# Kernel optimization log

Hardware: AMD Instinct MI355X
Metric: run time of the kernel (lower is better)

## Reference

```python
import jax, jax.numpy as jnp
import numpy as np

B, C, W, H = 4, 64, 64, 64
CQK = C // 8  # query/key channels


def setup_inputs() -> dict:
    key = jax.random.key(0)
    ks = jax.random.split(key, 8)
    s = 0.05
    return {
        "x": jax.random.normal(ks[0], (B, C, W, H), jnp.float32),
        "Wq": jax.random.normal(ks[1], (CQK, C), jnp.float32) * s,
        "bq": jax.random.normal(ks[2], (CQK,), jnp.float32) * s,
        "Wk": jax.random.normal(ks[3], (CQK, C), jnp.float32) * s,
        "bk": jax.random.normal(ks[4], (CQK,), jnp.float32) * s,
        "Wv": jax.random.normal(ks[5], (C, C), jnp.float32) * s,
        "bv": jax.random.normal(ks[6], (C,), jnp.float32) * s,
        # torch init is zeros; use a nonzero value so the attention path is exercised
        "gamma": jax.random.normal(ks[7], (1,), jnp.float32) * s,
    }


def reference(x, Wq, bq, Wk, bk, Wv, bv, gamma):
    b, c, w, h = x.shape
    n = w * h
    xf = x.reshape(b, c, n)  # B, C, N
    # 1x1 convs == per-pixel linear maps
    q = jnp.einsum("oc,bcn->bno", Wq, xf) + bq           # B, N, Cqk
    k = jnp.einsum("oc,bcn->bon", Wk, xf) + bk[:, None]   # B, Cqk, N
    energy = jnp.einsum("bno,bom->bnm", q, k)             # B, N, N
    attn = jax.nn.softmax(energy, axis=-1)                # B, N, N
    v = jnp.einsum("oc,bcn->bon", Wv, xf) + bv[:, None]   # B, C, N
    # out[b,c,j] = sum_n v[b,c,n] * attn[j,n]  (bmm with attention^T)
    out = jnp.einsum("bcn,bjn->bcj", v, attn)
    out = out.reshape(b, c, w, h)
    return gamma * out + x
```

## Files before the change

kernel.cpp:

```cpp
#include <hip/hip_runtime.h>

typedef short s16x8 __attribute__((ext_vector_type(8)));
typedef float f32x4 __attribute__((ext_vector_type(4)));
typedef float f32x16 __attribute__((ext_vector_type(16)));
typedef unsigned u32x4 __attribute__((ext_vector_type(4)));

#define BB 4
#define NN 4096
#define LOG2E 1.4426950408889634f

__device__ __forceinline__ unsigned short f2bf(float f) {
    unsigned int u = __builtin_bit_cast(unsigned int, f);
    u += 0x7fff + ((u >> 16) & 1);
    return (unsigned short)(u >> 16);
}

__device__ __forceinline__ unsigned pk2(float lo, float hi) {
    return __builtin_amdgcn_perm(__builtin_bit_cast(unsigned, hi),
                                 __builtin_bit_cast(unsigned, lo), 0x07060302u);
}

__device__ __forceinline__ void pl32swap(unsigned &a, unsigned &b) {
    asm volatile("v_permlane32_swap_b32 %0, %1" : "+v"(a), "+v"(b));
}

__global__ __launch_bounds__(256) void proj_kernel(
    const float* __restrict__ x,
    const float* __restrict__ Wq, const float* __restrict__ bq,
    const float* __restrict__ Wk, const float* __restrict__ bk,
    const float* __restrict__ Wv, const float* __restrict__ bv,
    unsigned short* __restrict__ Qw, unsigned short* __restrict__ Kw,
    unsigned short* __restrict__ Vc)
{
    __shared__ __attribute__((aligned(16))) unsigned short sW[80 * 72];
    __shared__ __attribute__((aligned(16))) unsigned short xT[64 * 72];
    __shared__ float sb[80];

    int tid = threadIdx.x;
    int p   = blockIdx.x;
    int xcd = p & 7;
    int b   = xcd >> 1;
    int nb  = ((p >> 3) << 1) | (xcd & 1);
    int n0  = nb << 6;

    for (int i = tid; i < 1280; i += 256) {
        int o = i >> 4, c4 = (i & 15) << 2;
        const float* src = (o < 8) ? &Wq[o * 64 + c4]
                         : ((o < 16) ? &Wk[(o - 8) * 64 + c4]
                                     : &Wv[(o - 16) * 64 + c4]);
        float4 v = *(const float4*)src;
        float sc = (o < 8) ? LOG2E : 1.f;
        sW[o * 72 + c4 + 0] = f2bf(v.x * sc);
        sW[o * 72 + c4 + 1] = f2bf(v.y * sc);
        sW[o * 72 + c4 + 2] = f2bf(v.z * sc);
        sW[o * 72 + c4 + 3] = f2bf(v.w * sc);
    }
    if (tid < 80)
        sb[tid] = (tid < 8) ? bq[tid] * LOG2E
                            : ((tid < 16) ? bk[tid - 8] : bv[tid - 16]);
    for (int i = tid; i < 1024; i += 256) {
        int c = i >> 4, p4 = (i & 15) << 2;
        float4 v = *(const float4*)&x[(((size_t)b * 64 + c) << 12) + n0 + p4];
        xT[(p4 + 0) * 72 + c] = f2bf(v.x);
        xT[(p4 + 1) * 72 + c] = f2bf(v.y);
        xT[(p4 + 2) * 72 + c] = f2bf(v.z);
        xT[(p4 + 3) * 72 + c] = f2bf(v.w);
    }
    __syncthreads();

    int w = tid >> 6, l = tid & 63, g = l >> 4, q16 = l & 15;
    int pix = w * 16 + q16;

    s16x8 bf0 = *(const s16x8*)&xT[pix * 72 + g * 8];
    s16x8 bf1 = *(const s16x8*)&xT[pix * 72 + 32 + g * 8];

    s16x8 a0[5], a1[5];
#pragma unroll
    for (int ot = 0; ot < 5; ++ot) {
        a0[ot] = *(const s16x8*)&sW[(ot * 16 + q16) * 72 + g * 8];
        a1[ot] = *(const s16x8*)&sW[(ot * 16 + q16) * 72 + 32 + g * 8];
    }
    __syncthreads();

    unsigned short* sV = xT;
    size_t base16 = ((size_t)(b << 12) + n0 + pix) << 4;

#pragma unroll
    for (int ot = 0; ot < 5; ++ot) {
        f32x4 acc = {0.f, 0.f, 0.f, 0.f};
        acc = __builtin_amdgcn_mfma_f32_16x16x32_bf16(a0[ot], bf0, acc, 0, 0, 0);
        acc = __builtin_amdgcn_mfma_f32_16x16x32_bf16(a1[ot], bf1, acc, 0, 0, 0);
#pragma unroll
        for (int r = 0; r < 4; ++r) {
            int orow = ot * 16 + g * 4 + r;
            unsigned short hv = f2bf(acc[r] + sb[orow]);
            if (ot == 0) {
                if (orow < 8) {
                    Qw[base16 + orow] = hv;
                    Qw[base16 + orow + 8] = 0;
                } else {
                    Kw[base16 + orow - 8] = hv;
                    Kw[base16 + orow] = 0;
                }
            } else {
                sV[(orow - 16) * 72 + pix] = hv;
            }
        }
    }
    __syncthreads();

#pragma unroll
    for (int i = tid; i < 512; i += 256) {
        int jj = i >> 6, c = i & 63;
        u32x4 v = *(const u32x4*)&sV[c * 72 + jj * 8];
        int jglob = (nb << 3) + jj;
        *(u32x4*)&Vc[(((size_t)b * 512 + jglob) * 64 + c) * 8] = v;
    }
}

__global__ __launch_bounds__(512, 2) void attn_kernel(
    const unsigned short* __restrict__ Qw, const unsigned short* __restrict__ Kw,
    const unsigned short* __restrict__ Vc, const float* __restrict__ x,
    const float* __restrict__ gamma, float* __restrict__ outp)
{
    __shared__ __attribute__((aligned(16))) float sO[64 * 36];
    __shared__ float sL[8 * 32];
    __shared__ float sGL[32];

    int tid = threadIdx.x;
    int w = tid >> 6, l = tid & 63, r31 = l & 31, hi = l >> 5;
    int p = blockIdx.x;
    int xcd = p & 7, kgrp = p >> 3;
    int b = xcd >> 1;
    int n32 = (kgrp & 1) | ((xcd & 1) << 1) | ((kgrp >> 1) << 2);
    int n0 = n32 << 5;
    float gm = gamma[0];

    s16x8 qf = *(const s16x8*)((const char*)Qw + ((size_t)b << 17)
                               + ((size_t)(n0 + r31) << 5) + (hi << 4));
    const char* KbW = (const char*)Kw + ((size_t)b << 17) + (w << 14)
                    + (r31 << 5) + (hi << 4);
    const char* VcB = (const char*)Vc + ((size_t)b << 19) + (w << 16)
                    + (hi << 10) + (r31 << 4);

    f32x16 zz;
#pragma unroll
    for (int i = 0; i < 16; ++i) zz[i] = 0.f;

    f32x16 acc0, acc1;
#pragma unroll
    for (int i = 0; i < 16; ++i) { acc0[i] = 0.f; acc1[i] = 0.f; }
    float la = 0.f;

    s16x8 cK  = *(const s16x8*)(KbW);
    s16x8 cA0 = *(const s16x8*)(VcB);
    s16x8 cA1 = *(const s16x8*)(VcB + 2048);
    s16x8 cB0 = *(const s16x8*)(VcB + 512);
    s16x8 cB1 = *(const s16x8*)(VcB + 2560);

#pragma unroll
    for (int ch = 0; ch < 16; ++ch) {
        s16x8 nK = cK, nA0 = cA0, nA1 = cA1, nB0 = cB0, nB1 = cB1;
        if (ch < 15) {
            const char* pk = KbW + ((ch + 1) << 10);
            const char* pv = VcB + ((ch + 1) << 12);
            nK  = *(const s16x8*)(pk);
            nA0 = *(const s16x8*)(pv);
            nA1 = *(const s16x8*)(pv + 2048);
            nB0 = *(const s16x8*)(pv + 512);
            nB1 = *(const s16x8*)(pv + 2560);
        }

        f32x16 E = __builtin_amdgcn_mfma_f32_32x32x16_bf16(cK, qf, zz, 0, 0, 0);
#pragma unroll
        for (int i = 0; i < 16; ++i) E[i] = __builtin_amdgcn_exp2f(E[i]);
        la += (((E[0] + E[1]) + (E[2] + E[3])) + ((E[4] + E[5]) + (E[6] + E[7])))
            + (((E[8] + E[9]) + (E[10] + E[11])) + ((E[12] + E[13]) + (E[14] + E[15])));

        unsigned x0 = pk2(E[0], E[1]),   x1 = pk2(E[2], E[3]);
        unsigned x2 = pk2(E[4], E[5]),   x3 = pk2(E[6], E[7]);
        unsigned x4 = pk2(E[8], E[9]),   x5 = pk2(E[10], E[11]);
        unsigned x6 = pk2(E[12], E[13]), x7 = pk2(E[14], E[15]);
        pl32swap(x0, x2); pl32swap(x1, x3);
        pl32swap(x4, x6); pl32swap(x5, x7);
        u32x4 u0 = {x0, x1, x2, x3}, u1 = {x4, x5, x6, x7};
        s16x8 pf0 = __builtin_bit_cast(s16x8, u0);
        s16x8 pf1 = __builtin_bit_cast(s16x8, u1);

        acc0 = __builtin_amdgcn_mfma_f32_32x32x16_bf16(cA0, pf0, acc0, 0, 0, 0);
        acc0 = __builtin_amdgcn_mfma_f32_32x32x16_bf16(cA1, pf1, acc0, 0, 0, 0);
        acc1 = __builtin_amdgcn_mfma_f32_32x32x16_bf16(cB0, pf0, acc1, 0, 0, 0);
        acc1 = __builtin_amdgcn_mfma_f32_32x32x16_bf16(cB1, pf1, acc1, 0, 0, 0);

        cK = nK; cA0 = nA0; cA1 = nA1; cB0 = nB0; cB1 = nB1;
    }

    la += __shfl_xor(la, 32);
    if (l < 32) sL[w * 32 + l] = la;

#pragma unroll
    for (int s = 0; s < 8; ++s) {
        __syncthreads();
#pragma unroll
        for (int B = 0; B < 8; ++B) {
            if (((w + s) & 7) == B) {
                const int R2 = B & 3;
                float e0 = (B < 4) ? acc0[R2 * 4 + 0] : acc1[R2 * 4 + 0];
                float e1 = (B < 4) ? acc0[R2 * 4 + 1] : acc1[R2 * 4 + 1];
                float e2 = (B < 4) ? acc0[R2 * 4 + 2] : acc1[R2 * 4 + 2];
                float e3 = (B < 4) ? acc0[R2 * 4 + 3] : acc1[R2 * 4 + 3];
                float* pp = &sO[(B * 8 + hi * 4) * 36 + r31];
                if (s == 0) {
                    pp[0] = e0; pp[36] = e1; pp[72] = e2; pp[108] = e3;
                } else {
                    pp[0] += e0; pp[36] += e1; pp[72] += e2; pp[108] += e3;
                }
            }
        }
    }
    __syncthreads();

    if (tid < 32) {
        float L = 0.f;
#pragma unroll
        for (int wk2 = 0; wk2 < 8; ++wk2) L += sL[wk2 * 32 + tid];
        sGL[tid] = gm / L;
    }
    __syncthreads();

    {
        int c = tid >> 3, qc = tid & 7;
        float4 o4 = *(const float4*)&sO[c * 36 + qc * 4];
        float4 g4 = *(const float4*)&sGL[qc * 4];
        size_t idx = (((size_t)b * 64 + c) << 12) + n0 + qc * 4;
        float4 x4v = *(const float4*)&x[idx];
        o4.x = o4.x * g4.x + x4v.x;
        o4.y = o4.y * g4.y + x4v.y;
        o4.z = o4.z * g4.z + x4v.z;
        o4.w = o4.w * g4.w + x4v.w;
        *(float4*)&outp[idx] = o4;
    }
}

extern "C" void kernel_launch(void* const* d_in, const int* in_sizes, int n_in,
                              void* d_out, int out_size, void* d_ws, size_t ws_size,
                              hipStream_t stream) {
    const float* x     = (const float*)d_in[0];
    const float* Wq    = (const float*)d_in[1];
    const float* bq    = (const float*)d_in[2];
    const float* Wk    = (const float*)d_in[3];
    const float* bk    = (const float*)d_in[4];
    const float* Wv    = (const float*)d_in[5];
    const float* bv    = (const float*)d_in[6];
    const float* gamma = (const float*)d_in[7];
    float* out = (float*)d_out;

    unsigned short* Qw = (unsigned short*)d_ws;
    unsigned short* Kw = Qw + (size_t)BB * NN * 16;
    unsigned short* Vc = Kw + (size_t)BB * NN * 16;

    proj_kernel<<<256, 256, 0, stream>>>(x, Wq, bq, Wk, bk, Wv, bv, Qw, Kw, Vc);
    attn_kernel<<<512, 512, 0, stream>>>(Qw, Kw, Vc, x, gamma, out);
}
```

Before: 29.35 us.

## Switch attention to 16-query tiles with 16x16x32 MFMA and more blocks

Each attention block now handles 16 queries instead of 32, using 16x16x32 bf16 MFMAs and doubling the grid to 1024 blocks. Launch bounds move to 6 blocks per CU, and the loop is no longer unrolled or software-prefetched. The goal is more parallelism and occupancy so latency is hidden by other waves rather than explicit prefetch. The cost is that K/V are re-read twice as often per query, and QK MFMAs waste three quarters of their lanes on zero-padded Q/K fragments.

```diff
diff --git a/kernel.cpp b/kernel.cpp
--- a/kernel.cpp
+++ b/kernel.cpp
@@ -2,7 +2,6 @@
 
 typedef short s16x8 __attribute__((ext_vector_type(8)));
 typedef float f32x4 __attribute__((ext_vector_type(4)));
-typedef float f32x16 __attribute__((ext_vector_type(16)));
 typedef unsigned u32x4 __attribute__((ext_vector_type(4)));
 
 #define BB 4
@@ -18,10 +17,6 @@
 __device__ __forceinline__ unsigned pk2(float lo, float hi) {
     return __builtin_amdgcn_perm(__builtin_bit_cast(unsigned, hi),
                                  __builtin_bit_cast(unsigned, lo), 0x07060302u);
-}
-
-__device__ __forceinline__ void pl32swap(unsigned &a, unsigned &b) {
-    asm volatile("v_permlane32_swap_b32 %0, %1" : "+v"(a), "+v"(b));
 }
 
 __global__ __launch_bounds__(256) void proj_kernel(
@@ -118,127 +113,115 @@
     }
 }
 
-__global__ __launch_bounds__(512, 2) void attn_kernel(
+__global__ __launch_bounds__(512, 6) void attn_kernel(
     const unsigned short* __restrict__ Qw, const unsigned short* __restrict__ Kw,
     const unsigned short* __restrict__ Vc, const float* __restrict__ x,
     const float* __restrict__ gamma, float* __restrict__ outp)
 {
-    __shared__ __attribute__((aligned(16))) float sO[64 * 36];
-    __shared__ float sL[8 * 32];
-    __shared__ float sGL[32];
+    __shared__ __attribute__((aligned(16))) float sO[64 * 17];
+    __shared__ float sL[8 * 16];
+    __shared__ float sGL[16];
 
     int tid = threadIdx.x;
-    int w = tid >> 6, l = tid & 63, r31 = l & 31, hi = l >> 5;
+    int w = tid >> 6, l = tid & 63, g = l >> 4, q16 = l & 15;
     int p = blockIdx.x;
-    int xcd = p & 7, kgrp = p >> 3;
+    int xcd = p & 7;
     int b = xcd >> 1;
-    int n32 = (kgrp & 1) | ((xcd & 1) << 1) | ((kgrp >> 1) << 2);
-    int n0 = n32 << 5;
+    int hi5 = (p >> 3) >> 2, lo2 = (p >> 3) & 3;
+    int qg = (hi5 << 3) | ((xcd & 1) << 2) | lo2;
+    int n0 = qg << 4;
     float gm = gamma[0];
 
-    s16x8 qf = *(const s16x8*)((const char*)Qw + ((size_t)b << 17)
-                               + ((size_t)(n0 + r31) << 5) + (hi << 4));
-    const char* KbW = (const char*)Kw + ((size_t)b << 17) + (w << 14)
-                    + (r31 << 5) + (hi << 4);
-    const char* VcB = (const char*)Vc + ((size_t)b << 19) + (w << 16)
-                    + (hi << 10) + (r31 << 4);
-
-    f32x16 zz;
-#pragma unroll
-    for (int i = 0; i < 16; ++i) zz[i] = 0.f;
-
-    f32x16 acc0, acc1;
-#pragma unroll
-    for (int i = 0; i < 16; ++i) { acc0[i] = 0.f; acc1[i] = 0.f; }
+    s16x8 z8 = {0, 0, 0, 0, 0, 0, 0, 0};
+    f32x4 z4 = {0.f, 0.f, 0.f, 0.f};
+
+    s16x8 qf = z8;
+    if (g == 0)
+        qf = *(const s16x8*)((const char*)Qw + ((size_t)b << 17)
+                             + ((size_t)(n0 + q16) << 5));
+
+    const char* Kb = (const char*)Kw + ((size_t)b << 17) + (w << 14)
+                   + ((((q16 >> 2) << 3) + (q16 & 3)) << 5);
+    const char* Vb = (const char*)Vc + ((size_t)b << 19) + (w << 16)
+                   + (g << 10) + (q16 << 4);
+
+    f32x4 acc0 = z4, acc1 = z4, acc2 = z4, acc3 = z4;
     float la = 0.f;
 
-    s16x8 cK  = *(const s16x8*)(KbW);
-    s16x8 cA0 = *(const s16x8*)(VcB);
-    s16x8 cA1 = *(const s16x8*)(VcB + 2048);
-    s16x8 cB0 = *(const s16x8*)(VcB + 512);
-    s16x8 cB1 = *(const s16x8*)(VcB + 2560);
-
-#pragma unroll
+#pragma unroll 1
     for (int ch = 0; ch < 16; ++ch) {
-        s16x8 nK = cK, nA0 = cA0, nA1 = cA1, nB0 = cB0, nB1 = cB1;
-        if (ch < 15) {
-            const char* pk = KbW + ((ch + 1) << 10);
-            const char* pv = VcB + ((ch + 1) << 12);
-            nK  = *(const s16x8*)(pk);
-            nA0 = *(const s16x8*)(pv);
-            nA1 = *(const s16x8*)(pv + 2048);
-            nB0 = *(const s16x8*)(pv + 512);
-            nB1 = *(const s16x8*)(pv + 2560);
+        const char* kc = Kb + (ch << 10);
+        s16x8 kf0 = z8, kf1 = z8;
+        if (g == 0) {
+            kf0 = *(const s16x8*)(kc);
+            kf1 = *(const s16x8*)(kc + 128);
         }
-
-        f32x16 E = __builtin_amdgcn_mfma_f32_32x32x16_bf16(cK, qf, zz, 0, 0, 0);
-#pragma unroll
-        for (int i = 0; i < 16; ++i) E[i] = __builtin_amdgcn_exp2f(E[i]);
-        la += (((E[0] + E[1]) + (E[2] + E[3])) + ((E[4] + E[5]) + (E[6] + E[7])))
-            + (((E[8] + E[9]) + (E[10] + E[11])) + ((E[12] + E[13]) + (E[14] + E[15])));
-
-        unsigned x0 = pk2(E[0], E[1]),   x1 = pk2(E[2], E[3]);
-        unsigned x2 = pk2(E[4], E[5]),   x3 = pk2(E[6], E[7]);
-        unsigned x4 = pk2(E[8], E[9]),   x5 = pk2(E[10], E[11]);
-        unsigned x6 = pk2(E[12], E[13]), x7 = pk2(E[14], E[15]);
-        pl32swap(x0, x2); pl32swap(x1, x3);
-        pl32swap(x4, x6); pl32swap(x5, x7);
-        u32x4 u0 = {x0, x1, x2, x3}, u1 = {x4, x5, x6, x7};
-        s16x8 pf0 = __builtin_bit_cast(s16x8, u0);
-        s16x8 pf1 = __builtin_bit_cast(s16x8, u1);
-
-        acc0 = __builtin_amdgcn_mfma_f32_32x32x16_bf16(cA0, pf0, acc0, 0, 0, 0);
-        acc0 = __builtin_amdgcn_mfma_f32_32x32x16_bf16(cA1, pf1, acc0, 0, 0, 0);
-        acc1 = __builtin_amdgcn_mfma_f32_32x32x16_bf16(cB0, pf0, acc1, 0, 0, 0);
-        acc1 = __builtin_amdgcn_mfma_f32_32x32x16_bf16(cB1, pf1, acc1, 0, 0, 0);
-
-        cK = nK; cA0 = nA0; cA1 = nA1; cB0 = nB0; cB1 = nB1;
-    }
-
+        const char* vc = Vb + (ch << 12);
+        s16x8 vf0 = *(const s16x8*)(vc);
+        s16x8 vf1 = *(const s16x8*)(vc + 256);
+        s16x8 vf2 = *(const s16x8*)(vc + 512);
+        s16x8 vf3 = *(const s16x8*)(vc + 768);
+
+        f32x4 E0 = __builtin_amdgcn_mfma_f32_16x16x32_bf16(kf0, qf, z4, 0, 0, 0);
+        f32x4 E1 = __builtin_amdgcn_mfma_f32_16x16x32_bf16(kf1, qf, z4, 0, 0, 0);
+#pragma unroll
+        for (int i = 0; i < 4; ++i) E0[i] = __builtin_amdgcn_exp2f(E0[i]);
+#pragma unroll
+        for (int i = 0; i < 4; ++i) E1[i] = __builtin_amdgcn_exp2f(E1[i]);
+        la += ((E0[0] + E0[1]) + (E0[2] + E0[3]))
+            + ((E1[0] + E1[1]) + (E1[2] + E1[3]));
+
+        u32x4 uu = { pk2(E0[0], E0[1]), pk2(E0[2], E0[3]),
+                     pk2(E1[0], E1[1]), pk2(E1[2], E1[3]) };
+        s16x8 pf = __builtin_bit_cast(s16x8, uu);
+
+        acc0 = __builtin_amdgcn_mfma_f32_16x16x32_bf16(vf0, pf, acc0, 0, 0, 0);
+        acc1 = __builtin_amdgcn_mfma_f32_16x16x32_bf16(vf1, pf, acc1, 0, 0, 0);
+        acc2 = __builtin_amdgcn_mfma_f32_16x16x32_bf16(vf2, pf, acc2, 0, 0, 0);
+        acc3 = __builtin_amdgcn_mfma_f32_16x16x32_bf16(vf3, pf, acc3, 0, 0, 0);
+    }
+
+    la += __shfl_xor(la, 16);
     la += __shfl_xor(la, 32);
-    if (l < 32) sL[w * 32 + l] = la;
+    if (l < 16) sL[w * 16 + l] = la;
 
 #pragma unroll
     for (int s = 0; s < 8; ++s) {
         __syncthreads();
 #pragma unroll
         for (int B = 0; B < 8; ++B) {
-            if (((w + s) & 7) == B) {
-                const int R2 = B & 3;
-                float e0 = (B < 4) ? acc0[R2 * 4 + 0] : acc1[R2 * 4 + 0];
-                float e1 = (B < 4) ? acc0[R2 * 4 + 1] : acc1[R2 * 4 + 1];
-                float e2 = (B < 4) ? acc0[R2 * 4 + 2] : acc1[R2 * 4 + 2];
-                float e3 = (B < 4) ? acc0[R2 * 4 + 3] : acc1[R2 * 4 + 3];
-                float* pp = &sO[(B * 8 + hi * 4) * 36 + r31];
+            if (((w + s) & 7) == B && ((g >> 1) == (B & 1))) {
+                const int CT = B >> 1;
+                f32x4 e = (CT == 0) ? acc0 : ((CT == 1) ? acc1
+                        : ((CT == 2) ? acc2 : acc3));
+                float* pp = &sO[(CT * 16 + g * 4) * 17 + q16];
                 if (s == 0) {
-                    pp[0] = e0; pp[36] = e1; pp[72] = e2; pp[108] = e3;
+                    pp[0] = e[0]; pp[17] = e[1]; pp[34] = e[2]; pp[51] = e[3];
                 } else {
-                    pp[0] += e0; pp[36] += e1; pp[72] += e2; pp[108] += e3;
+                    pp[0] += e[0]; pp[17] += e[1]; pp[34] += e[2]; pp[51] += e[3];
                 }
             }
         }
     }
     __syncthreads();
 
-    if (tid < 32) {
+    if (tid < 16) {
         float L = 0.f;
 #pragma unroll
-        for (int wk2 = 0; wk2 < 8; ++wk2) L += sL[wk2 * 32 + tid];
+        for (int w2 = 0; w2 < 8; ++w2) L += sL[w2 * 16 + tid];
         sGL[tid] = gm / L;
     }
     __syncthreads();
 
     {
-        int c = tid >> 3, qc = tid & 7;
-        float4 o4 = *(const float4*)&sO[c * 36 + qc * 4];
-        float4 g4 = *(const float4*)&sGL[qc * 4];
-        size_t idx = (((size_t)b * 64 + c) << 12) + n0 + qc * 4;
-        float4 x4v = *(const float4*)&x[idx];
-        o4.x = o4.x * g4.x + x4v.x;
-        o4.y = o4.y * g4.y + x4v.y;
-        o4.z = o4.z * g4.z + x4v.z;
-        o4.w = o4.w * g4.w + x4v.w;
-        *(float4*)&outp[idx] = o4;
+        int c = tid >> 3, j = tid & 7;
+        int q = j * 2;
+        size_t idx = (((size_t)b * 64 + c) << 12) + n0 + q;
+        float2 x2 = *(const float2*)&x[idx];
+        float o0 = sGL[q] * sO[c * 17 + q] + x2.x;
+        float o1 = sGL[q + 1] * sO[c * 17 + q + 1] + x2.y;
+        float2 o2 = {o0, o1};
+        *(float2*)&outp[idx] = o2;
     }
 }
 
@@ -260,5 +243,5 @@
     unsigned short* Vc = Kw + (size_t)BB * NN * 16;
 
     proj_kernel<<<256, 256, 0, stream>>>(x, Wq, bq, Wk, bk, Wv, bv, Qw, Kw, Vc);
-    attn_kernel<<<512, 512, 0, stream>>>(Qw, Kw, Vc, x, gamma, out);
-}
+    attn_kernel<<<1024, 512, 0, stream>>>(Qw, Kw, Vc, x, gamma, out);
+}
```

Measured after the change: 37.48 us. 1.28x slower.
